# Optimization experiments

Measured on AMD Instinct MI355X. Metric: run time of the kernel, lower is better.

Reference implementation:

```python
import jax, jax.numpy as jnp
import numpy as np

N = 50000   # nodes
E = 800000  # edges (avg degree 16)
F = 96      # num_features
H = 96      # hidden_channels
G = 64      # graphs in batch
ALPHA = 0.5


def setup_inputs() -> dict:
    key = jax.random.key(0)
    ks = jax.random.split(key, 32)
    inp = {
        "x": jax.random.normal(ks[0], (N, F), jnp.float32),
        "edge_index": jax.random.randint(ks[1], (2, E), 0, N, dtype=jnp.int32),
        "batch": jnp.sort(jax.random.randint(ks[2], (N,), 0, G, dtype=jnp.int32)),
    }
    i = 3
    dims = [(F, H), (H, H), (H, H)]
    for l, (din, dout) in enumerate(dims, start=1):
        for tag in ("Wself", "Wsd", "Wds"):
            inp[f"{tag}{l}"] = jax.random.normal(ks[i], (din, dout), jnp.float32) * 0.05; i += 1
        for tag in ("bself", "bsd", "bds"):
            inp[f"{tag}{l}"] = jax.random.normal(ks[i], (dout,), jnp.float32) * 0.05; i += 1
    inp["lin1_w"] = jax.random.normal(ks[i], (H, 5), jnp.float32) * 0.05; i += 1
    inp["lin1_b"] = jax.random.normal(ks[i], (5,), jnp.float32) * 0.05; i += 1
    inp["lin2_w"] = jax.random.normal(ks[i], (5, 1), jnp.float32) * 0.05; i += 1
    inp["lin2_b"] = jax.random.normal(ks[i], (1,), jnp.float32) * 0.05
    return inp


def _agg_mean(x, idx_from, idx_to, n):
    # scatter-mean of x[idx_from] onto idx_to (PyG SAGEConv mean aggregation;
    # nodes with no incoming edges get 0)
    s = jax.ops.segment_sum(x[idx_from], idx_to, num_segments=n)
    c = jax.ops.segment_sum(jnp.ones((idx_to.shape[0],), x.dtype), idx_to, num_segments=n)
    return s / jnp.maximum(c, 1.0)[:, None]


def _dir_sage(x, src, dst, Wself, bself, Wsd, bsd, Wds, bds):
    n = x.shape[0]
    out_self = x @ Wself + bself
    # source_to_target: aggregate x[src] at dst; target_to_source: aggregate x[dst] at src
    out_sd = _agg_mean(x, src, dst, n) @ Wsd + bsd
    out_ds = _agg_mean(x, dst, src, n) @ Wds + bds
    return out_self + (1.0 - ALPHA) * out_sd + ALPHA * out_ds


def reference(x, edge_index, batch,
              Wself1, bself1, Wsd1, bsd1, Wds1, bds1,
              Wself2, bself2, Wsd2, bsd2, Wds2, bds2,
              Wself3, bself3, Wsd3, bsd3, Wds3, bds3,
              lin1_w, lin1_b, lin2_w, lin2_b):
    src, dst = edge_index[0], edge_index[1]
    h = jax.nn.relu(_dir_sage(x, src, dst, Wself1, bself1, Wsd1, bsd1, Wds1, bds1))
    h = jax.nn.relu(_dir_sage(h, src, dst, Wself2, bself2, Wsd2, bsd2, Wds2, bds2))
    h = jax.nn.relu(_dir_sage(h, src, dst, Wself3, bself3, Wsd3, bsd3, Wds3, bds3))
    g = jax.ops.segment_max(h, batch, num_segments=G)  # global_max_pool -> [G, H]
    g = jax.nn.relu(g @ lin1_w + lin1_b)
    return g @ lin2_w + lin2_b  # [G, 1]
```

## Files before the change

kernel.cpp:

```cpp
#include <hip/hip_runtime.h>
#include <hip/hip_bf16.h>

#define HF 96
#define GG 64
#define DEG 64
#define CAPB 4608
#define CPAD 100

typedef __attribute__((ext_vector_type(8))) short bf16x8;
typedef __attribute__((ext_vector_type(4))) float f32x4;
typedef __attribute__((ext_vector_type(4))) unsigned int uint4v;
typedef unsigned int uint;

union BFU { uint4v u; bf16x8 b; };

__device__ __forceinline__ unsigned short f2bf(float f) {
    unsigned u = __float_as_uint(f);
    unsigned r = (u + 0x7FFFu + ((u >> 16) & 1u)) >> 16;
    return (unsigned short)r;
}
__device__ __forceinline__ float bf2f(unsigned short h) {
    return __uint_as_float(((unsigned)h) << 16);
}

__device__ __forceinline__ uint4 pack_hilo4(float f0, float f1, float f2, float f3) {
    unsigned short h0 = f2bf(f0), h1 = f2bf(f1), h2 = f2bf(f2), h3 = f2bf(f3);
    unsigned short l0 = f2bf(f0 - bf2f(h0)), l1 = f2bf(f1 - bf2f(h1));
    unsigned short l2 = f2bf(f2 - bf2f(h2)), l3 = f2bf(f3 - bf2f(h3));
    uint4 o;
    o.x = (uint)h0 | ((uint)h1 << 16);
    o.y = (uint)h2 | ((uint)h3 << 16);
    o.z = (uint)l0 | ((uint)l1 << 16);
    o.w = (uint)l2 | ((uint)l3 << 16);
    return o;
}

__device__ __forceinline__ void acc_hilo4(float4& a, uint4 w) {
    a.x += __uint_as_float(w.x << 16) + __uint_as_float(w.z << 16);
    a.y += __uint_as_float(w.x & 0xFFFF0000u) + __uint_as_float(w.z & 0xFFFF0000u);
    a.z += __uint_as_float(w.y << 16) + __uint_as_float(w.w << 16);
    a.w += __uint_as_float(w.y & 0xFFFF0000u) + __uint_as_float(w.w & 0xFFFF0000u);
}

__global__ __launch_bounds__(256) void build_phase1(
        const float* __restrict__ x, const int* __restrict__ ei,
        unsigned short* __restrict__ hbuf,
        uint* __restrict__ pcnt, uint* __restrict__ pq, unsigned* __restrict__ g,
        const float* Ws1, const float* Wsd1, const float* Wds1,
        const float* bs1, const float* bsd1, const float* bds1,
        const float* Ws2, const float* Wsd2, const float* Wds2,
        const float* bs2, const float* bsd2, const float* bds2,
        const float* Ws3, const float* Wsd3, const float* Wds3,
        const float* bs3, const float* bsd3, const float* bds3,
        unsigned short* __restrict__ Whi3, unsigned short* __restrict__ Wlo3,
        float* __restrict__ bc3, int N, int E, int NB, int CE) {
    if (blockIdx.x < 256) {
        __shared__ int hist[512];
        __shared__ int lbase[512];
        for (int i = threadIdx.x; i < NB; i += 256) hist[i] = 0;
        __syncthreads();
        const int e0 = blockIdx.x * CE;
        int e1 = e0 + CE; if (e1 > E) e1 = E;
        for (int e = e0 + threadIdx.x; e < e1; e += 256) {
            int s = ei[e], d = ei[E + e];
            atomicAdd(&hist[d >> 8], 1);
            atomicAdd(&hist[(N + s) >> 8], 1);
        }
        __syncthreads();
        for (int b = threadIdx.x; b < NB; b += 256) {
            int h = hist[b];
            lbase[b] = h ? (int)atomicAdd(&pcnt[b], (uint)h) : 0;
        }
        __syncthreads();
        for (int e = e0 + threadIdx.x; e < e1; e += 256) {
            int s = ei[e], d = ei[E + e];
            int b0 = d >> 8;
            int p0 = atomicAdd(&lbase[b0], 1);
            if (p0 < CAPB) pq[(long long)b0 * CAPB + p0] = ((uint)(d & 255) << 16) | (uint)s;
            int k1 = N + s;
            int b1 = k1 >> 8;
            int p1 = atomicAdd(&lbase[b1], 1);
            if (p1 < CAPB) pq[(long long)b1 * CAPB + p1] = ((uint)(k1 & 255) << 16) | (uint)d;
        }
        return;
    }
    int t = (blockIdx.x - 256) * 256 + threadIdx.x;
    const int R0 = N * 24;
    if (t < R0) {
        int n = t / 24, q = t % 24;
        float4 v = *(const float4*)(x + (long long)n * HF + q * 4);
        *(uint4*)(hbuf + ((long long)n * 192 + q * 8)) = pack_hilo4(v.x, v.y, v.z, v.w);
        return;
    }
    t -= R0;
    if (t < GG * HF) { g[t] = 0u; return; }
    t -= GG * HF;
    const int PER = HF * 288 + HF;
    if (t >= 3 * PER) return;
    int l = t / PER;
    int idx = t % PER;
    const float* Wself = (l == 0) ? Ws1 : (l == 1) ? Ws2 : Ws3;
    const float* Wsd   = (l == 0) ? Wsd1 : (l == 1) ? Wsd2 : Wsd3;
    const float* Wds   = (l == 0) ? Wds1 : (l == 1) ? Wds2 : Wds3;
    const float* bself = (l == 0) ? bs1 : (l == 1) ? bs2 : bs3;
    const float* bsd   = (l == 0) ? bsd1 : (l == 1) ? bsd2 : bsd3;
    const float* bds   = (l == 0) ? bds1 : (l == 1) ? bds2 : bds3;
    unsigned short* Whi = Whi3 + (long long)l * HF * 288;
    unsigned short* Wlo = Wlo3 + (long long)l * HF * 288;
    float* bc = bc3 + l * HF;
    if (idx < HF * 288) {
        int j = idx / 288;
        int kk = idx % 288;
        int m = kk / HF, k = kk % HF;
        const float* W = (m == 0) ? Wself : (m == 1) ? Wsd : Wds;
        float w = W[k * HF + j];
        unsigned short hi = f2bf(w);
        Whi[idx] = hi;
        Wlo[idx] = f2bf(w - bf2f(hi));
    } else {
        int j = idx - HF * 288;
        bc[j] = bself[j] + 0.5f * (bsd[j] + bds[j]);
    }
}

__global__ __launch_bounds__(256) void build_phase2(
        const uint* __restrict__ pcnt, const uint* __restrict__ pq,
        int* __restrict__ cnt, int* __restrict__ nbr, int N) {
    int b = blockIdx.x;
    __shared__ int lcnt[256];
    lcnt[threadIdx.x] = 0;
    __syncthreads();
    int tot = (int)pcnt[b]; if (tot > CAPB) tot = CAPB;
    const uint* q = pq + (long long)b * CAPB;
    for (int i = threadIdx.x; i < tot; i += 256) {
        uint p = q[i];
        int lk = (int)(p >> 16);
        int v = (int)(p & 0xFFFFu);
        int slot = atomicAdd(&lcnt[lk], 1);
        long long k = ((long long)b << 8) + lk;
        if (slot < DEG) nbr[(k << 6) + slot] = v;
    }
    __syncthreads();
    long long k = ((long long)b << 8) + threadIdx.x;
    if (k < 2LL * N) cnt[k] = lcnt[threadIdx.x];
}

__global__ __launch_bounds__(256) void gather_kernel(
        const unsigned short* __restrict__ hbuf, unsigned short* __restrict__ abuf,
        const int* __restrict__ cnt, const int* __restrict__ nbr, int N) {
    int t = blockIdx.x * blockDim.x + threadIdx.x;
    int P = t / 24;
    if (P >= 2 * N) return;
    int q = t % 24;
    int dir = (P >= N) ? 1 : 0;
    int n = P - dir * N;

    int degt = cnt[P];
    int deg = (degt > DEG) ? DEG : degt;
    const int* nb = nbr + ((long long)P << 6);

    const unsigned short* xq = hbuf + q * 8;
    float4 a0 = make_float4(0.f, 0.f, 0.f, 0.f);
    float4 a1 = a0, a2 = a0, a3 = a0;
    int i = 0;
    for (; i + 4 <= deg; i += 4) {
        int i0 = nb[i + 0], i1 = nb[i + 1], i2 = nb[i + 2], i3 = nb[i + 3];
        uint4 w0 = *(const uint4*)(xq + (long long)i0 * 192);
        uint4 w1 = *(const uint4*)(xq + (long long)i1 * 192);
        uint4 w2 = *(const uint4*)(xq + (long long)i2 * 192);
        uint4 w3 = *(const uint4*)(xq + (long long)i3 * 192);
        acc_hilo4(a0, w0);
        acc_hilo4(a1, w1);
        acc_hilo4(a2, w2);
        acc_hilo4(a3, w3);
    }
    for (; i < deg; i++) {
        uint4 w0 = *(const uint4*)(xq + (long long)nb[i] * 192);
        acc_hilo4(a0, w0);
    }
    float4 acc;
    acc.x = (a0.x + a1.x) + (a2.x + a3.x);
    acc.y = (a0.y + a1.y) + (a2.y + a3.y);
    acc.z = (a0.z + a1.z) + (a2.z + a3.z);
    acc.w = (a0.w + a1.w) + (a2.w + a3.w);
    float inv = 0.5f / fmaxf((float)degt, 1.0f);
    acc.x *= inv; acc.y *= inv; acc.z *= inv; acc.w *= inv;
    *(uint4*)(abuf + ((long long)n * 384 + (dir * 24 + q) * 8)) =
        pack_hilo4(acc.x, acc.y, acc.z, acc.w);
}

__global__ __launch_bounds__(256) void sage_mfma(
        const unsigned short* __restrict__ hbuf, const unsigned short* __restrict__ abuf,
        unsigned short* __restrict__ hout,
        const unsigned short* __restrict__ Whi_g, const unsigned short* __restrict__ Wlo_g,
        const float* __restrict__ bc, const int* __restrict__ batch,
        unsigned* __restrict__ gmax, int mode, int N) {
    __shared__ __align__(16) float C[64 * CPAD];

    const int tx = threadIdx.x;
    const int lane = tx & 63;
    const int wid = tx >> 6;
    const int wr = (wid >> 1) * 32;
    const int wc = (wid & 1) * 48;
    const int m = lane & 15;
    const int quad = lane >> 4;
    const int row0 = blockIdx.x * 64;

    int rA[2];
#pragma unroll
    for (int rt = 0; rt < 2; rt++) {
        int r = row0 + wr + rt * 16 + m;
        rA[rt] = (r < N) ? r : (N - 1);
    }
    const unsigned short* hrow0 = hbuf + (long long)rA[0] * 192;
    const unsigned short* hrow1 = hbuf + (long long)rA[1] * 192;
    const unsigned short* arow0 = abuf + (long long)rA[0] * 384;
    const unsigned short* arow1 = abuf + (long long)rA[1] * 384;
    long long wbase[3];
#pragma unroll
    for (int ct = 0; ct < 3; ct++) wbase[ct] = (long long)(wc + ct * 16 + m) * 288 + quad * 8;

    f32x4 acc[2][3];
#pragma unroll
    for (int rt = 0; rt < 2; rt++)
#pragma unroll
        for (int ct = 0; ct < 3; ct++) acc[rt][ct] = (f32x4){0.f, 0.f, 0.f, 0.f};

#define KSTEP(PA0, PA1, KOFF) do {                                                   \
    bf16x8 ah[2], al[2], bh[3], bl[3];                                               \
    { uint4 v0 = *(const uint4*)(PA0); uint4 v1 = *(const uint4*)((PA0) + 8);        \
      BFU uh; uh.u = (uint4v){v0.x, v0.y, v1.x, v1.y}; ah[0] = uh.b;                 \
      BFU ul; ul.u = (uint4v){v0.z, v0.w, v1.z, v1.w}; al[0] = ul.b; }               \
    { uint4 v0 = *(const uint4*)(PA1); uint4 v1 = *(const uint4*)((PA1) + 8);        \
      BFU uh; uh.u = (uint4v){v0.x, v0.y, v1.x, v1.y}; ah[1] = uh.b;                 \
      BFU ul; ul.u = (uint4v){v0.z, v0.w, v1.z, v1.w}; al[1] = ul.b; }               \
    _Pragma("unroll")                                                                \
    for (int ct = 0; ct < 3; ct++) {                                                 \
        bh[ct] = *(const bf16x8*)(Whi_g + wbase[ct] + (KOFF));                       \
        bl[ct] = *(const bf16x8*)(Wlo_g + wbase[ct] + (KOFF));                       \
    }                                                                                \
    _Pragma("unroll")                                                                \
    for (int rt = 0; rt < 2; rt++)                                                   \
        _Pragma("unroll")                                                            \
        for (int ct = 0; ct < 3; ct++) {                                             \
            acc[rt][ct] = __builtin_amdgcn_mfma_f32_16x16x32_bf16(ah[rt], bh[ct], acc[rt][ct], 0, 0, 0); \
            acc[rt][ct] = __builtin_amdgcn_mfma_f32_16x16x32_bf16(ah[rt], bl[ct], acc[rt][ct], 0, 0, 0); \
            acc[rt][ct] = __builtin_amdgcn_mfma_f32_16x16x32_bf16(al[rt], bh[ct], acc[rt][ct], 0, 0, 0); \
        }                                                                            \
} while (0)

#pragma unroll
    for (int kt = 0; kt < 3; kt++)
        KSTEP(hrow0 + (kt * 8 + quad * 2) * 8, hrow1 + (kt * 8 + quad * 2) * 8, kt * 32);
#pragma unroll
    for (int kt = 0; kt < 3; kt++)
        KSTEP(arow0 + (kt * 8 + quad * 2) * 8, arow1 + (kt * 8 + quad * 2) * 8, 96 + kt * 32);
#pragma unroll
    for (int kt = 0; kt < 3; kt++)
        KSTEP(arow0 + 192 + (kt * 8 + quad * 2) * 8, arow1 + 192 + (kt * 8 + quad * 2) * 8,
              192 + kt * 32);
#undef KSTEP

#pragma unroll
    for (int ct = 0; ct < 3; ct++) {
        int col = wc + ct * 16 + m;
        float bcv = bc[col];
#pragma unroll
        for (int rt = 0; rt < 2; rt++) {
#pragma unroll
            for (int reg = 0; reg < 4; reg++) {
                int rl = wr + rt * 16 + quad * 4 + reg;
                C[rl * CPAD + col] = fmaxf(acc[rt][ct][reg] + bcv, 0.f);
            }
        }
    }
    __syncthreads();

    if (mode == 0) {
        int rl = tx >> 2;
        int aj = tx & 3;
        int r = row0 + rl;
        if (r < N) {
            unsigned short* Orow = hout + (long long)r * 192;
#pragma unroll
            for (int k = 0; k < 6; k++) {
                int c = aj * 6 + k;
                const float* src = &C[rl * CPAD + c * 4];
                *(uint4*)(Orow + c * 8) = pack_hilo4(src[0], src[1], src[2], src[3]);
            }
        }
    } else {
        if (tx < HF) {
            int j = tx;
            int rmax = N - row0; if (rmax > 64) rmax = 64;
            float cur = 0.0f;
            int curb = -1;
            for (int r = 0; r < rmax; r++) {
                int bt = batch[row0 + r];
                float v = C[r * CPAD + j];
                if (bt != curb) {
                    if (curb >= 0) atomicMax(&gmax[curb * HF + j], __float_as_uint(cur));
                    curb = bt;
                    cur = v;
                } else {
                    cur = fmaxf(cur, v);
                }
            }
            if (curb >= 0) atomicMax(&gmax[curb * HF + j], __float_as_uint(cur));
        }
    }
}

__global__ void mlp_kernel(const unsigned* __restrict__ g, const float* __restrict__ lin1_w,
                           const float* __restrict__ lin1_b, const float* __restrict__ lin2_w,
                           const float* __restrict__ lin2_b, float* __restrict__ out) {
    int gi = threadIdx.x;
    if (gi >= GG) return;
    float h5[5];
#pragma unroll
    for (int hh = 0; hh < 5; hh++) {
        float acc = lin1_b[hh];
#pragma unroll 8
        for (int k = 0; k < HF; k++)
            acc = fmaf(__uint_as_float(g[gi * HF + k]), lin1_w[k * 5 + hh], acc);
        h5[hh] = fmaxf(acc, 0.0f);
    }
    float o = lin2_b[0];
#pragma unroll
    for (int hh = 0; hh < 5; hh++) o = fmaf(h5[hh], lin2_w[hh * 1 + 0], o);
    out[gi] = o;
}

extern "C" void kernel_launch(void* const* d_in, const int* in_sizes, int n_in,
                              void* d_out, int out_size, void* d_ws, size_t ws_size,
                              hipStream_t stream) {
    const float* x     = (const float*)d_in[0];
    const int*   ei    = (const int*)d_in[1];
    const int*   batch = (const int*)d_in[2];
    const float* W[3][3];
    const float* B[3][3];
    for (int l = 0; l < 3; l++) {
        for (int t = 0; t < 3; t++) W[l][t] = (const float*)d_in[3 + l * 6 + t];
        for (int t = 0; t < 3; t++) B[l][t] = (const float*)d_in[3 + l * 6 + 3 + t];
    }
    const float* lin1_w = (const float*)d_in[21];
    const float* lin1_b = (const float*)d_in[22];
    const float* lin2_w = (const float*)d_in[23];
    const float* lin2_b = (const float*)d_in[24];

    const int N = in_sizes[0] / HF;
    const int E = in_sizes[1] / 2;
    const int NB = (2 * N + 255) / 256;
    const int CE = (E + 255) / 256;

    unsigned short* hbuf = (unsigned short*)d_ws;
    unsigned short* abuf = hbuf + (long long)N * 192;
    int* cnt = (int*)(abuf + (long long)N * 384);
    int* nbr = cnt + 2LL * N;
    uint* pcnt = (uint*)(nbr + 2LL * N * DEG);
    uint* pq = pcnt + NB;
    float* bc3 = (float*)(pq + (long long)NB * CAPB);
    uintptr_t p = (uintptr_t)(bc3 + 3 * HF);
    p = (p + 15) & ~(uintptr_t)15;
    unsigned short* Whi3 = (unsigned short*)p;
    unsigned short* Wlo3 = Whi3 + 3 * HF * 288;
    uintptr_t p2 = (uintptr_t)(Wlo3 + 3 * HF * 288);
    p2 = (p2 + 15) & ~(uintptr_t)15;
    unsigned* g = (unsigned*)p2;

    hipMemsetAsync(pcnt, 0, (size_t)NB * sizeof(uint), stream);

    const long long lin_threads = (long long)N * 24 + GG * HF + 3LL * (HF * 288 + HF);
    const int lin_blocks = (int)((lin_threads + 255) / 256);
    build_phase1<<<256 + lin_blocks, 256, 0, stream>>>(
        x, ei, hbuf, pcnt, pq, g,
        W[0][0], W[0][1], W[0][2], B[0][0], B[0][1], B[0][2],
        W[1][0], W[1][1], W[1][2], B[1][0], B[1][1], B[1][2],
        W[2][0], W[2][1], W[2][2], B[2][0], B[2][1], B[2][2],
        Whi3, Wlo3, bc3, N, E, NB, CE);
    build_phase2<<<NB, 256, 0, stream>>>(pcnt, pq, cnt, nbr, N);

    const long long gather_threads = (long long)2 * N * 24;
    const int gather_blocks = (int)((gather_threads + 255) / 256);
    const int gemm_blocks = (N + 63) / 64;

    for (int l = 0; l < 3; l++) {
        gather_kernel<<<gather_blocks, 256, 0, stream>>>(hbuf, abuf, cnt, nbr, N);
        sage_mfma<<<gemm_blocks, 256, 0, stream>>>(
            hbuf, abuf, hbuf,
            Whi3 + (long long)l * HF * 288, Wlo3 + (long long)l * HF * 288,
            bc3 + l * HF, batch, g, (l < 2) ? 0 : 1, N);
    }

    mlp_kernel<<<1, 64, 0, stream>>>(g, lin1_w, lin1_b, lin2_w, lin2_b, (float*)d_out);
}
```

Before: 499.7 us.

## Stage activation and weight tiles through double-buffered LDS in sage_mfma

The SAGE MFMA kernel used to have each wave load activation rows and hi/lo weight fragments straight from global memory every k-step, so weights were fetched redundantly by each wave. It now loads A (hi/lo split) and W tiles cooperatively into a double-buffered shared-memory pool with padded rows, prefetching the next k-step into registers while the current step's MFMAs run. This cuts redundant global weight traffic and overlaps loads with compute, at the cost of more LDS use (lower occupancy) and a barrier per k-step.

```diff
diff --git a/kernel.cpp b/kernel.cpp
--- a/kernel.cpp
+++ b/kernel.cpp
@@ -6,13 +6,11 @@
 #define DEG 64
 #define CAPB 4608
 #define CPAD 100
+#define LPAD 40
 
 typedef __attribute__((ext_vector_type(8))) short bf16x8;
 typedef __attribute__((ext_vector_type(4))) float f32x4;
-typedef __attribute__((ext_vector_type(4))) unsigned int uint4v;
 typedef unsigned int uint;
-
-union BFU { uint4v u; bf16x8 b; };
 
 __device__ __forceinline__ unsigned short f2bf(float f) {
     unsigned u = __float_as_uint(f);
@@ -195,7 +193,8 @@
         const unsigned short* __restrict__ Whi_g, const unsigned short* __restrict__ Wlo_g,
         const float* __restrict__ bc, const int* __restrict__ batch,
         unsigned* __restrict__ gmax, int mode, int N) {
-    __shared__ __align__(16) float C[64 * CPAD];
+    __shared__ __align__(16) unsigned short POOL[2 * 12800];
+    float* C = (float*)POOL;
 
     const int tx = threadIdx.x;
     const int lane = tx & 63;
@@ -206,19 +205,52 @@
     const int quad = lane >> 4;
     const int row0 = blockIdx.x * 64;
 
-    int rA[2];
-#pragma unroll
-    for (int rt = 0; rt < 2; rt++) {
-        int r = row0 + wr + rt * 16 + m;
-        rA[rt] = (r < N) ? r : (N - 1);
-    }
-    const unsigned short* hrow0 = hbuf + (long long)rA[0] * 192;
-    const unsigned short* hrow1 = hbuf + (long long)rA[1] * 192;
-    const unsigned short* arow0 = abuf + (long long)rA[0] * 384;
-    const unsigned short* arow1 = abuf + (long long)rA[1] * 384;
-    long long wbase[3];
-#pragma unroll
-    for (int ct = 0; ct < 3; ct++) wbase[ct] = (long long)(wc + ct * 16 + m) * 288 + quad * 8;
+    const int ar0 = tx >> 3, aj0 = tx & 7;
+    const int ar1 = (tx + 256) >> 3;
+    int garc0 = row0 + ar0; if (garc0 > N - 1) garc0 = N - 1;
+    int garc1 = row0 + ar1; if (garc1 > N - 1) garc1 = N - 1;
+
+    const int w1_lo = (tx + 256) >= 384;
+    const int w1_idx = w1_lo ? (tx + 256 - 384) : (tx + 256);
+    const int w2_idx = tx + 128;
+
+    uint4 ra0, ra1, rw0, rw1, rw2;
+
+#define LOAD_REGS(KT) do {                                                            \
+    const unsigned short *sa0, *sa1;                                                  \
+    if ((KT) < 3) {                                                                   \
+        sa0 = hbuf + (long long)garc0 * 192 + ((KT) * 8 + aj0) * 8;                   \
+        sa1 = hbuf + (long long)garc1 * 192 + ((KT) * 8 + aj0) * 8;                   \
+    } else if ((KT) < 6) {                                                            \
+        sa0 = abuf + (long long)garc0 * 384 + (((KT) - 3) * 8 + aj0) * 8;             \
+        sa1 = abuf + (long long)garc1 * 384 + (((KT) - 3) * 8 + aj0) * 8;             \
+    } else {                                                                          \
+        sa0 = abuf + (long long)garc0 * 384 + 192 + (((KT) - 6) * 8 + aj0) * 8;       \
+        sa1 = abuf + (long long)garc1 * 384 + 192 + (((KT) - 6) * 8 + aj0) * 8;       \
+    }                                                                                 \
+    ra0 = *(const uint4*)sa0;                                                         \
+    ra1 = *(const uint4*)sa1;                                                         \
+    const int kg = (KT) * 32;                                                         \
+    rw0 = *(const uint4*)(Whi_g + (long long)(tx >> 2) * 288 + kg + (tx & 3) * 8);    \
+    { const unsigned short* Wg = w1_lo ? Wlo_g : Whi_g;                               \
+      rw1 = *(const uint4*)(Wg + (long long)(w1_idx >> 2) * 288 + kg + (w1_idx & 3) * 8); } \
+    rw2 = *(const uint4*)(Wlo_g + (long long)(w2_idx >> 2) * 288 + kg + (w2_idx & 3) * 8); \
+} while (0)
+
+#define WRITE_LDS(B) do {                                                             \
+    unsigned short* Ahi = (B);                                                        \
+    unsigned short* Alo = (B) + 2560;                                                 \
+    unsigned short* Whs = (B) + 5120;                                                 \
+    unsigned short* Wls = (B) + 8960;                                                 \
+    *(uint2*)&Ahi[ar0 * LPAD + aj0 * 4] = make_uint2(ra0.x, ra0.y);                   \
+    *(uint2*)&Alo[ar0 * LPAD + aj0 * 4] = make_uint2(ra0.z, ra0.w);                   \
+    *(uint2*)&Ahi[ar1 * LPAD + aj0 * 4] = make_uint2(ra1.x, ra1.y);                   \
+    *(uint2*)&Alo[ar1 * LPAD + aj0 * 4] = make_uint2(ra1.z, ra1.w);                   \
+    *(uint4*)&Whs[(tx >> 2) * LPAD + (tx & 3) * 8] = rw0;                             \
+    { unsigned short* Wd = w1_lo ? Wls : Whs;                                         \
+      *(uint4*)&Wd[(w1_idx >> 2) * LPAD + (w1_idx & 3) * 8] = rw1; }                  \
+    *(uint4*)&Wls[(w2_idx >> 2) * LPAD + (w2_idx & 3) * 8] = rw2;                     \
+} while (0)
 
     f32x4 acc[2][3];
 #pragma unroll
@@ -226,40 +258,50 @@
 #pragma unroll
         for (int ct = 0; ct < 3; ct++) acc[rt][ct] = (f32x4){0.f, 0.f, 0.f, 0.f};
 
-#define KSTEP(PA0, PA1, KOFF) do {                                                   \
-    bf16x8 ah[2], al[2], bh[3], bl[3];                                               \
-    { uint4 v0 = *(const uint4*)(PA0); uint4 v1 = *(const uint4*)((PA0) + 8);        \
-      BFU uh; uh.u = (uint4v){v0.x, v0.y, v1.x, v1.y}; ah[0] = uh.b;                 \
-      BFU ul; ul.u = (uint4v){v0.z, v0.w, v1.z, v1.w}; al[0] = ul.b; }               \
-    { uint4 v0 = *(const uint4*)(PA1); uint4 v1 = *(const uint4*)((PA1) + 8);        \
-      BFU uh; uh.u = (uint4v){v0.x, v0.y, v1.x, v1.y}; ah[1] = uh.b;                 \
-      BFU ul; ul.u = (uint4v){v0.z, v0.w, v1.z, v1.w}; al[1] = ul.b; }               \
-    _Pragma("unroll")                                                                \
-    for (int ct = 0; ct < 3; ct++) {                                                 \
-        bh[ct] = *(const bf16x8*)(Whi_g + wbase[ct] + (KOFF));                       \
-        bl[ct] = *(const bf16x8*)(Wlo_g + wbase[ct] + (KOFF));                       \
-    }                                                                                \
-    _Pragma("unroll")                                                                \
-    for (int rt = 0; rt < 2; rt++)                                                   \
-        _Pragma("unroll")                                                            \
-        for (int ct = 0; ct < 3; ct++) {                                             \
-            acc[rt][ct] = __builtin_amdgcn_mfma_f32_16x16x32_bf16(ah[rt], bh[ct], acc[rt][ct], 0, 0, 0); \
-            acc[rt][ct] = __builtin_amdgcn_mfma_f32_16x16x32_bf16(ah[rt], bl[ct], acc[rt][ct], 0, 0, 0); \
-            acc[rt][ct] = __builtin_amdgcn_mfma_f32_16x16x32_bf16(al[rt], bh[ct], acc[rt][ct], 0, 0, 0); \
-        }                                                                            \
-} while (0)
-
-#pragma unroll
-    for (int kt = 0; kt < 3; kt++)
-        KSTEP(hrow0 + (kt * 8 + quad * 2) * 8, hrow1 + (kt * 8 + quad * 2) * 8, kt * 32);
-#pragma unroll
-    for (int kt = 0; kt < 3; kt++)
-        KSTEP(arow0 + (kt * 8 + quad * 2) * 8, arow1 + (kt * 8 + quad * 2) * 8, 96 + kt * 32);
-#pragma unroll
-    for (int kt = 0; kt < 3; kt++)
-        KSTEP(arow0 + 192 + (kt * 8 + quad * 2) * 8, arow1 + 192 + (kt * 8 + quad * 2) * 8,
-              192 + kt * 32);
-#undef KSTEP
+    LOAD_REGS(0);
+    WRITE_LDS(POOL);
+    __syncthreads();
+
+    for (int kt = 0; kt < 9; kt++) {
+        if (kt < 8) LOAD_REGS(kt + 1);
+
+        unsigned short* B = POOL + (kt & 1) * 12800;
+        unsigned short* Ahi = B;
+        unsigned short* Alo = B + 2560;
+        unsigned short* Whs = B + 5120;
+        unsigned short* Wls = B + 8960;
+
+        bf16x8 ah[2], al[2], bh[3], bl[3];
+#pragma unroll
+        for (int rt = 0; rt < 2; rt++) {
+            int r = (wr + rt * 16 + m) * LPAD + quad * 8;
+            ah[rt] = *(const bf16x8*)&Ahi[r];
+            al[rt] = *(const bf16x8*)&Alo[r];
+        }
+#pragma unroll
+        for (int ct = 0; ct < 3; ct++) {
+            int r = (wc + ct * 16 + m) * LPAD + quad * 8;
+            bh[ct] = *(const bf16x8*)&Whs[r];
+            bl[ct] = *(const bf16x8*)&Wls[r];
+        }
+#pragma unroll
+        for (int rt = 0; rt < 2; rt++)
+#pragma unroll
+            for (int ct = 0; ct < 3; ct++) {
+                acc[rt][ct] = __builtin_amdgcn_mfma_f32_16x16x32_bf16(ah[rt], bh[ct], acc[rt][ct], 0, 0, 0);
+                acc[rt][ct] = __builtin_amdgcn_mfma_f32_16x16x32_bf16(ah[rt], bl[ct], acc[rt][ct], 0, 0, 0);
+                acc[rt][ct] = __builtin_amdgcn_mfma_f32_16x16x32_bf16(al[rt], bh[ct], acc[rt][ct], 0, 0, 0);
+            }
+
+        if (kt < 8) {
+            WRITE_LDS(POOL + ((kt + 1) & 1) * 12800);
+            __syncthreads();
+        }
+    }
+    __syncthreads();
+
+#undef LOAD_REGS
+#undef WRITE_LDS
 
 #pragma unroll
     for (int ct = 0; ct < 3; ct++) {
```

Result: faster. 470.6 us (-5.8%).

## Stage A tiles through LDS with coalesced loads in sage_mfma

Applied to the files above, without the earlier changes.

The dense GEMM kernel now loads the 64-row block of packed hi/lo activations (self plus the two aggregated directions) cooperatively into two padded LDS arrays with coalesced 16-byte loads, deinterleaving hi and lo halves. The MFMA k-loop then reads A fragments from LDS instead of issuing scattered per-lane global loads and repacking in registers. The output tile C reuses the AH buffer, which needs an extra barrier, and launch bounds now request two blocks per CU. LDS use grows to about 76 KB per block, which may limit occupancy.

```diff
diff --git a/kernel.cpp b/kernel.cpp
--- a/kernel.cpp
+++ b/kernel.cpp
@@ -6,13 +6,11 @@
 #define DEG 64
 #define CAPB 4608
 #define CPAD 100
+#define APAD 296
 
 typedef __attribute__((ext_vector_type(8))) short bf16x8;
 typedef __attribute__((ext_vector_type(4))) float f32x4;
-typedef __attribute__((ext_vector_type(4))) unsigned int uint4v;
 typedef unsigned int uint;
-
-union BFU { uint4v u; bf16x8 b; };
 
 __device__ __forceinline__ unsigned short f2bf(float f) {
     unsigned u = __float_as_uint(f);
@@ -189,13 +187,15 @@
         pack_hilo4(acc.x, acc.y, acc.z, acc.w);
 }
 
-__global__ __launch_bounds__(256) void sage_mfma(
+__global__ __launch_bounds__(256, 2) void sage_mfma(
         const unsigned short* __restrict__ hbuf, const unsigned short* __restrict__ abuf,
         unsigned short* __restrict__ hout,
         const unsigned short* __restrict__ Whi_g, const unsigned short* __restrict__ Wlo_g,
         const float* __restrict__ bc, const int* __restrict__ batch,
         unsigned* __restrict__ gmax, int mode, int N) {
-    __shared__ __align__(16) float C[64 * CPAD];
+    __shared__ __align__(16) unsigned short AH[64 * APAD];
+    __shared__ __align__(16) unsigned short AL[64 * APAD];
+    float* C = (float*)AH;
 
     const int tx = threadIdx.x;
     const int lane = tx & 63;
@@ -206,60 +206,60 @@
     const int quad = lane >> 4;
     const int row0 = blockIdx.x * 64;
 
-    int rA[2];
-#pragma unroll
-    for (int rt = 0; rt < 2; rt++) {
-        int r = row0 + wr + rt * 16 + m;
-        rA[rt] = (r < N) ? r : (N - 1);
-    }
-    const unsigned short* hrow0 = hbuf + (long long)rA[0] * 192;
-    const unsigned short* hrow1 = hbuf + (long long)rA[1] * 192;
-    const unsigned short* arow0 = abuf + (long long)rA[0] * 384;
-    const unsigned short* arow1 = abuf + (long long)rA[1] * 384;
+    {
+        const int arow = tx >> 2;
+        const int aj = tx & 3;
+        int garc = row0 + arow; if (garc > N - 1) garc = N - 1;
+        const unsigned short* hrow = hbuf + (long long)garc * 192;
+        const unsigned short* grow = abuf + (long long)garc * 384;
+#pragma unroll
+        for (int cc = 0; cc < 18; cc++) {
+            int c = cc * 4 + aj;
+            const unsigned short* src = (c < 24) ? (hrow + c * 8) : (grow + (c - 24) * 8);
+            uint4 v = *(const uint4*)src;
+            *(uint2*)&AH[arow * APAD + c * 4] = make_uint2(v.x, v.y);
+            *(uint2*)&AL[arow * APAD + c * 4] = make_uint2(v.z, v.w);
+        }
+    }
+    __syncthreads();
+
+    f32x4 acc[2][3];
+#pragma unroll
+    for (int rt = 0; rt < 2; rt++)
+#pragma unroll
+        for (int ct = 0; ct < 3; ct++) acc[rt][ct] = (f32x4){0.f, 0.f, 0.f, 0.f};
+
+    int abase[2];
+#pragma unroll
+    for (int rt = 0; rt < 2; rt++) abase[rt] = (wr + rt * 16 + m) * APAD + quad * 8;
     long long wbase[3];
 #pragma unroll
     for (int ct = 0; ct < 3; ct++) wbase[ct] = (long long)(wc + ct * 16 + m) * 288 + quad * 8;
 
-    f32x4 acc[2][3];
-#pragma unroll
-    for (int rt = 0; rt < 2; rt++)
-#pragma unroll
-        for (int ct = 0; ct < 3; ct++) acc[rt][ct] = (f32x4){0.f, 0.f, 0.f, 0.f};
-
-#define KSTEP(PA0, PA1, KOFF) do {                                                   \
-    bf16x8 ah[2], al[2], bh[3], bl[3];                                               \
-    { uint4 v0 = *(const uint4*)(PA0); uint4 v1 = *(const uint4*)((PA0) + 8);        \
-      BFU uh; uh.u = (uint4v){v0.x, v0.y, v1.x, v1.y}; ah[0] = uh.b;                 \
-      BFU ul; ul.u = (uint4v){v0.z, v0.w, v1.z, v1.w}; al[0] = ul.b; }               \
-    { uint4 v0 = *(const uint4*)(PA1); uint4 v1 = *(const uint4*)((PA1) + 8);        \
-      BFU uh; uh.u = (uint4v){v0.x, v0.y, v1.x, v1.y}; ah[1] = uh.b;                 \
-      BFU ul; ul.u = (uint4v){v0.z, v0.w, v1.z, v1.w}; al[1] = ul.b; }               \
-    _Pragma("unroll")                                                                \
-    for (int ct = 0; ct < 3; ct++) {                                                 \
-        bh[ct] = *(const bf16x8*)(Whi_g + wbase[ct] + (KOFF));                       \
-        bl[ct] = *(const bf16x8*)(Wlo_g + wbase[ct] + (KOFF));                       \
-    }                                                                                \
-    _Pragma("unroll")                                                                \
-    for (int rt = 0; rt < 2; rt++)                                                   \
-        _Pragma("unroll")                                                            \
-        for (int ct = 0; ct < 3; ct++) {                                             \
-            acc[rt][ct] = __builtin_amdgcn_mfma_f32_16x16x32_bf16(ah[rt], bh[ct], acc[rt][ct], 0, 0, 0); \
-            acc[rt][ct] = __builtin_amdgcn_mfma_f32_16x16x32_bf16(ah[rt], bl[ct], acc[rt][ct], 0, 0, 0); \
-            acc[rt][ct] = __builtin_amdgcn_mfma_f32_16x16x32_bf16(al[rt], bh[ct], acc[rt][ct], 0, 0, 0); \
-        }                                                                            \
-} while (0)
-
-#pragma unroll
-    for (int kt = 0; kt < 3; kt++)
-        KSTEP(hrow0 + (kt * 8 + quad * 2) * 8, hrow1 + (kt * 8 + quad * 2) * 8, kt * 32);
-#pragma unroll
-    for (int kt = 0; kt < 3; kt++)
-        KSTEP(arow0 + (kt * 8 + quad * 2) * 8, arow1 + (kt * 8 + quad * 2) * 8, 96 + kt * 32);
-#pragma unroll
-    for (int kt = 0; kt < 3; kt++)
-        KSTEP(arow0 + 192 + (kt * 8 + quad * 2) * 8, arow1 + 192 + (kt * 8 + quad * 2) * 8,
-              192 + kt * 32);
-#undef KSTEP
+#pragma unroll 3
+    for (int kt = 0; kt < 9; kt++) {
+        const int kg = kt * 32;
+        bf16x8 ah[2], al[2], bh[3], bl[3];
+#pragma unroll
+        for (int rt = 0; rt < 2; rt++) {
+            ah[rt] = *(const bf16x8*)&AH[abase[rt] + kg];
+            al[rt] = *(const bf16x8*)&AL[abase[rt] + kg];
+        }
+#pragma unroll
+        for (int ct = 0; ct < 3; ct++) {
+            bh[ct] = *(const bf16x8*)(Whi_g + wbase[ct] + kg);
+            bl[ct] = *(const bf16x8*)(Wlo_g + wbase[ct] + kg);
+        }
+#pragma unroll
+        for (int rt = 0; rt < 2; rt++)
+#pragma unroll
+            for (int ct = 0; ct < 3; ct++) {
+                acc[rt][ct] = __builtin_amdgcn_mfma_f32_16x16x32_bf16(ah[rt], bh[ct], acc[rt][ct], 0, 0, 0);
+                acc[rt][ct] = __builtin_amdgcn_mfma_f32_16x16x32_bf16(ah[rt], bl[ct], acc[rt][ct], 0, 0, 0);
+                acc[rt][ct] = __builtin_amdgcn_mfma_f32_16x16x32_bf16(al[rt], bh[ct], acc[rt][ct], 0, 0, 0);
+            }
+    }
+    __syncthreads();
 
 #pragma unroll
     for (int ct = 0; ct < 3; ct++) {
```

Measured after the change: 475.9 us. 1.05x faster.
